# Optimization experiments

Hardware: AMD Instinct MI355X
Metric: run time of the kernel (lower is better)

The kernel has to match this reference:

```python
import jax, jax.numpy as jnp
import numpy as np

B, T, U = 64, 800, 96
VOCAB, CDIM, H, K, M = 80, 64, 400, 10, 20


def _lstm_cell(x, h, c, W_ih, W_hh, b_ih, b_hh):
    gates = x @ W_ih.T + h @ W_hh.T + b_ih + b_hh  # [B,4H]
    i, f, g, o = jnp.split(gates, 4, axis=-1)
    i, f, o = jax.nn.sigmoid(i), jax.nn.sigmoid(f), jax.nn.sigmoid(o)
    g = jnp.tanh(g)
    c = f * c + i * g
    h = o * jnp.tanh(c)
    return h, c


def setup_inputs() -> dict:
    key = jax.random.key(0)
    ks = jax.random.split(key, 16)
    s = 0.08
    emb = jax.random.normal(ks[0], (VOCAB, CDIM), jnp.float32) * s
    emb = emb.at[0].set(0.0)  # padding_idx=0
    d = {
        'x': jax.random.normal(ks[1], (B, T, 3), jnp.float32),
        'text_tokens': jax.random.randint(ks[2], (B, U), 0, VOCAB, jnp.int32),
        'emb': emb,
        'W_ih1': jax.random.normal(ks[3], (4 * H, 3 + CDIM), jnp.float32) * s,
        'W_hh1': jax.random.normal(ks[4], (4 * H, H), jnp.float32) * s,
        'b_ih1': jnp.zeros((4 * H,), jnp.float32),
        'b_hh1': jnp.zeros((4 * H,), jnp.float32),
        'W_ih2': jax.random.normal(ks[5], (4 * H, 3 + H + CDIM), jnp.float32) * s,
        'W_hh2': jax.random.normal(ks[6], (4 * H, H), jnp.float32) * s,
        'b_ih2': jnp.zeros((4 * H,), jnp.float32),
        'b_hh2': jnp.zeros((4 * H,), jnp.float32),
        'W_ih3': jax.random.normal(ks[7], (4 * H, 3 + H + CDIM), jnp.float32) * s,
        'W_hh3': jax.random.normal(ks[8], (4 * H, H), jnp.float32) * s,
        'b_ih3': jnp.zeros((4 * H,), jnp.float32),
        'b_hh3': jnp.zeros((4 * H,), jnp.float32),
        'W_w': jax.random.normal(ks[9], (3 * K, H), jnp.float32) * s,
        'b_w': jnp.concatenate([jnp.zeros((2 * K,), jnp.float32),
                                jnp.full((K,), -5.0, jnp.float32)]),
        'W_m': jax.random.normal(ks[10], (1 + 6 * M, 3 * H), jnp.float32) * s,
        'b_m': jnp.zeros((1 + 6 * M,), jnp.float32),
    }
    return d


def reference(x, text_tokens, emb, W_ih1, W_hh1, b_ih1, b_hh1,
              W_ih2, W_hh2, b_ih2, b_hh2, W_ih3, W_hh3, b_ih3, b_hh3,
              W_w, b_w, W_m, b_m):
    text_encoded = emb[text_tokens]  # [B,U,CDIM]
    u = jnp.arange(1, U + 1, dtype=jnp.float32)  # [U]

    z = jnp.zeros((B, H), jnp.float32)
    carry0 = (z, z, z, z, z, z,
              jnp.zeros((B, CDIM), jnp.float32),
              jnp.zeros((B, K), jnp.float32))

    def step(carry, x_t):
        h1, c1, h2, c2, h3, c3, w, kappa = carry
        h1, c1 = _lstm_cell(jnp.concatenate([x_t, w], -1), h1, c1,
                            W_ih1, W_hh1, b_ih1, b_hh1)
        # Gaussian window attention
        p = h1 @ W_w.T + b_w  # [B,3K]
        alpha_hat, beta_hat, kappa_hat = jnp.split(p, 3, axis=-1)
        alpha = jnp.exp(alpha_hat)
        beta = jnp.exp(beta_hat)
        kappa = kappa + jnp.exp(jnp.clip(kappa_hat, -10.0, 5.0))
        # phi: [B,U] = sum_k alpha * exp(-beta * (kappa - u)^2)
        diff = kappa[:, :, None] - u[None, None, :]  # [B,K,U]
        phi = jnp.sum(alpha[:, :, None] * jnp.exp(-beta[:, :, None] * diff * diff), axis=1)
        w = jnp.einsum('bu,bud->bd', phi, text_encoded)
        h2, c2 = _lstm_cell(jnp.concatenate([x_t, h1, w], -1), h2, c2,
                            W_ih2, W_hh2, b_ih2, b_hh2)
        h3, c3 = _lstm_cell(jnp.concatenate([x_t, h2, w], -1), h3, c3,
                            W_ih3, W_hh3, b_ih3, b_hh3)
        res = jnp.concatenate([h1, h2, h3], -1) @ W_m.T + b_m  # [B,1+6M]
        return (h1, c1, h2, c2, h3, c3, w, kappa), res

    _, res = jax.lax.scan(step, carry0, jnp.swapaxes(x, 0, 1))  # [T,B,1+6M]
    res = jnp.swapaxes(res, 0, 1)  # [B,T,1+6M]

    eos_hat = res[..., 0:1]
    pi = jax.nn.softmax(res[..., 1:1 + M], axis=-1)
    mu_x = res[..., 1 + M:1 + 2 * M]
    mu_y = res[..., 1 + 2 * M:1 + 3 * M]
    sigma_x = jnp.exp(res[..., 1 + 3 * M:1 + 4 * M]) + 1e-6
    sigma_y = jnp.exp(res[..., 1 + 4 * M:1 + 5 * M]) + 1e-6
    rho = jnp.tanh(res[..., 1 + 5 * M:1 + 6 * M]) * 0.999
    return (eos_hat, pi, mu_x, mu_y, sigma_x, sigma_y, rho)
```

## Files before the change

### kernel.cpp

```cpp
#include <hip/hip_runtime.h>


#define DI __device__ __forceinline__

typedef _Float16 f16;
typedef _Float16 f16x8 __attribute__((ext_vector_type(8)));
typedef _Float16 f16x4 __attribute__((ext_vector_type(4)));
typedef float f32x4 __attribute__((ext_vector_type(4)));
typedef unsigned long long u64;
typedef unsigned u32;

constexpr int Tn = 800, Un = 96, Hn = 400;
constexpr int P1 = 520, P2 = 904, P3 = 904, PM = 1288;
constexpr int NWG = 99;
constexpr int SP = 272;

constexpr size_t OFF_W1 = 0;
constexpr size_t SZ_W1 = (size_t)1600 * P1 * 2;
constexpr size_t OFF_W2 = OFF_W1 + SZ_W1;
constexpr size_t SZ_W2 = (size_t)1600 * P2 * 2;
constexpr size_t OFF_W3 = OFF_W2 + SZ_W2;
constexpr size_t OFF_WM = OFF_W3 + SZ_W2;
constexpr size_t SZ_WM = (size_t)128 * PM * 2;
constexpr size_t OFF_A1 = OFF_WM + SZ_WM;
constexpr size_t SZ_A1 = (size_t)2 * 64 * P1 * 2;
constexpr size_t OFF_A2 = OFF_A1 + SZ_A1;
constexpr size_t SZ_A2 = (size_t)2 * 64 * P2 * 2;
constexpr size_t OFF_A3 = OFF_A2 + SZ_A2;
constexpr size_t OFF_AM = OFF_A3 + SZ_A2;
constexpr size_t SZ_AM = (size_t)4 * 64 * PM * 2;
constexpr size_t OFF_TEB = OFF_AM + SZ_AM;
constexpr size_t SZ_TEB = (size_t)64 * 96 * 64 * 2;
constexpr size_t OFF_BS1 = OFF_TEB + SZ_TEB;
constexpr size_t OFF_BS2 = OFF_BS1 + 6400;
constexpr size_t OFF_BS3 = OFF_BS2 + 6400;
constexpr size_t OFF_BW = OFF_BS3 + 6400;
constexpr size_t OFF_BM = OFF_BW + 128;
constexpr size_t OFF_FLG = OFF_BM + 512;
constexpr size_t SZ_FLG = (size_t)808 * 5 * 16 * 4;
constexpr size_t OFF_PB = OFF_FLG + 24576;
constexpr size_t OFF_RES = OFF_FLG + SZ_FLG;

constexpr size_t O_EOS = 0, O_PI = 51200, O_MUX = 1075200, O_MUY = 2099200;
constexpr size_t O_SX = 3123200, O_SY = 4147200, O_RHO = 5171200;

constexpr int SB_L1 = 0;
constexpr int SB_ATT = 32;
constexpr int SB_L2 = 64;
constexpr int SB_L3 = 96;
constexpr int SB_OUT = 128;
constexpr int NSLOT = 160;

constexpr int GUARD_FLAG = 1200000;

DI u64 ldU8(const f16* p) {
  return __hip_atomic_load((const u64*)p, __ATOMIC_RELAXED, __HIP_MEMORY_SCOPE_AGENT);
}
DI void stU8(f16* p, u64 u) {
  __hip_atomic_store((u64*)p, u, __ATOMIC_RELAXED, __HIP_MEMORY_SCOPE_AGENT);
}
DI void stU8u(void* p, u64 u) {
  __hip_atomic_store((u64*)p, u, __ATOMIC_RELAXED, __HIP_MEMORY_SCOPE_AGENT);
}
DI u32 ldU4(const u32* p) {
  return __hip_atomic_load(p, __ATOMIC_RELAXED, __HIP_MEMORY_SCOPE_AGENT);
}
DI void stA4(f16* p, f16x4 v) {
  union { f16x4 v; u64 u; } c; c.v = v;
  stU8(p, c.u);
}
DI u64 pkf(float a, float b) {
  return (u64)__builtin_bit_cast(u32, a) | ((u64)__builtin_bit_cast(u32, b) << 32);
}

DI float sigm(float v) {
  return __builtin_amdgcn_rcpf(1.f + __expf(-v));
}
DI float ftanh(float v) {
  const float a = fabsf(v);
  const float e = __expf(-2.f * a);
  const float m = (1.f - e) * __builtin_amdgcn_rcpf(1.f + e);
  return v < 0.f ? -m : m;
}

DI void waitR(int* sl, int* doom,
              int b0, int n0, int q0, int b1, int n1, int q1,
              int b2, int n2, int q2, int b3, int n3, int q3) {
  if (!*doom) {
    if (threadIdx.x < 64) {
      const int l = (int)threadIdx.x;
      int sA = -1, qA = 0, sB = -1, qB = 0;
      {
        int idx = l;
        if (idx < n0) { sA = b0 + idx; qA = q0; }
        else { idx -= n0;
          if (idx < n1) { sA = b1 + idx; qA = q1; }
          else { idx -= n1;
            if (idx < n2) { sA = b2 + idx; qA = q2; }
            else { idx -= n2;
              if (idx < n3) { sA = b3 + idx; qA = q3; } } } }
      }
      {
        int idx = l + 64;
        if (idx < n0) { sB = b0 + idx; qB = q0; }
        else { idx -= n0;
          if (idx < n1) { sB = b1 + idx; qB = q1; }
          else { idx -= n1;
            if (idx < n2) { sB = b2 + idx; qB = q2; }
            else { idx -= n2;
              if (idx < n3) { sB = b3 + idx; qB = q3; } } } }
      }
      int okA = (sA < 0) ? 1 : 0, okB = (sB < 0) ? 1 : 0;
      int guard = 0;
      for (;;) {
        if (!okA)
          okA = (__hip_atomic_load(sl + sA * 32, __ATOMIC_RELAXED, __HIP_MEMORY_SCOPE_AGENT) >= qA) ? 1 : 0;
        if (!okB)
          okB = (__hip_atomic_load(sl + sB * 32, __ATOMIC_RELAXED, __HIP_MEMORY_SCOPE_AGENT) >= qB) ? 1 : 0;
        if (__all(okA & okB)) break;
        __builtin_amdgcn_s_sleep(1);
        if (++guard > GUARD_FLAG) { if (l == 0) *doom = 1; break; }
      }
    }
  }
  __syncthreads();
}
DI void arriveS(int* sl, int slot, int t) {
  __syncthreads();
  if (threadIdx.x == 0)
    __hip_atomic_store(sl + slot * 32, t, __ATOMIC_RELAXED, __HIP_MEMORY_SCOPE_AGENT);
}

template <int KN, int PITCH_>
DI void stage_ld(const f16* Ain, int tid, u64* lo, u64* hi) {
#pragma unroll
  for (int j = 0; j < KN; ++j) {
    const int i = tid + j * 256;
    const int r = i / (KN * 4), c16 = i % (KN * 4);
    const f16* p = Ain + (size_t)r * PITCH_ + c16 * 8;
    lo[j] = ldU8(p);
    hi[j] = ldU8(p + 4);
  }
}
template <int KN>
DI void stage_wr(f16* stg, int tid, const u64* lo, const u64* hi) {
#pragma unroll
  for (int j = 0; j < KN; ++j) {
    const int i = tid + j * 256;
    const int r = i / (KN * 4), c16 = i % (KN * 4);
    u64* q = (u64*)(stg + r * SP + c16 * 8);
    q[0] = lo[j];
    q[1] = hi[j];
  }
}
template <int KN>
DI void mfma_blk(const f16x8* wr, const f16* stg, int quad, int ln16, f32x4 acc[4]) {
#pragma unroll
  for (int ksl = 0; ksl < KN; ++ksl) {
    const int kc = ksl * 32 + quad * 8;
#pragma unroll
    for (int mt = 0; mt < 4; ++mt) {
      const f16x8 a = *(const f16x8*)(stg + (mt * 16 + ln16) * SP + kc);
      acc[mt] = __builtin_amdgcn_mfma_f32_16x16x32_f16(a, wr[ksl], acc[mt], 0, 0, 0);
    }
  }
}

DI void stage_ks14_ld(const f16* Ap, int pitch, const float* x, int t, int tid,
                      u64& sp, float& x0, float& x1, float& x2) {
  const int r = tid >> 2, cc = (tid & 3) * 4;
  sp = ldU8(Ap + (size_t)r * pitch + 448 + cc);
  if (tid < 64) {
    const float* xp = x + ((size_t)tid * Tn + t) * 3;
    x0 = xp[0]; x1 = xp[1]; x2 = xp[2];
  } else { x0 = x1 = x2 = 0.f; }
}
DI void stage_ks14_wr(f16* stg, int tid, u64 sp, float x0, float x1, float x2) {
  const int r = tid >> 2, cc = (tid & 3) * 4;
  *(u64*)(stg + r * SP + 128 + cc) = sp;
  if (tid < 64) {
    union { f16 h[4]; u64 u; } cx;
    cx.h[0] = (f16)x0; cx.h[1] = (f16)x1; cx.h[2] = (f16)x2; cx.h[3] = (f16)0.f;
    *(u64*)(stg + tid * SP + 144) = cx.u;
    *(u64*)(stg + tid * SP + 148) = 0ull;
    *(u64*)(stg + tid * SP + 152) = 0ull;
    *(u64*)(stg + tid * SP + 156) = 0ull;
  }
}

DI void gate_finish(f32x4 acc[4], float* red, float* cst, const float* bL, int tid,
                    int quad, int ln16, int wave,
                    f16* dA, int pA, f16* dB, int pB, f16* dC, int pC) {
#pragma unroll
  for (int mt = 0; mt < 4; ++mt)
#pragma unroll
    for (int r = 0; r < 4; ++r)
      red[wave * 1024 + (mt * 16 + quad * 4 + r) * 16 + ln16] = acc[mt][r];
  __syncthreads();
  {
    const int oi = tid * 4, b = oi >> 4, j0 = oi & 15;
    f32x4 gi = *(f32x4*)&red[oi];
    f32x4 gf = *(f32x4*)&red[1024 + oi];
    f32x4 gg = *(f32x4*)&red[2048 + oi];
    f32x4 go = *(f32x4*)&red[3072 + oi];
    f32x4 c = *(f32x4*)&cst[oi];
    f16x4 hv;
#pragma unroll
    for (int e = 0; e < 4; ++e) {
      const float iv = sigm(gi[e] + bL[j0 + e]);
      const float fv = sigm(gf[e] + bL[16 + j0 + e]);
      const float gv = ftanh(gg[e] + bL[32 + j0 + e]);
      const float ov = sigm(go[e] + bL[48 + j0 + e]);
      const float cn = fv * c[e] + iv * gv;
      c[e] = cn;
      hv[e] = (f16)(ov * ftanh(cn));
    }
    *(f32x4*)&cst[oi] = c;
    stA4(dA + b * pA + j0, hv);
    stA4(dB + b * pB + j0, hv);
    if (dC != nullptr) stA4(dC + b * pC + j0, hv);
  }
}

DI void gate_finish_l1(f32x4 acc[4], float* red, float* cst, const float* bL,
                       const float* wwL, int tid, int quad, int ln16, int wave,
                       u32* PBu, int jb,
                       f16* dA, int pA, f16* dB, int pB, f16* dC, int pC) {
#pragma unroll
  for (int mt = 0; mt < 4; ++mt)
#pragma unroll
    for (int r = 0; r < 4; ++r)
      red[wave * 1024 + (mt * 16 + quad * 4 + r) * 16 + ln16] = acc[mt][r];
  __syncthreads();
  const int oi = tid * 4, b = oi >> 4, j0 = oi & 15;
  f32x4 gi = *(f32x4*)&red[oi];
  f32x4 gf = *(f32x4*)&red[1024 + oi];
  f32x4 gg = *(f32x4*)&red[2048 + oi];
  f32x4 go = *(f32x4*)&red[3072 + oi];
  f32x4 c = *(f32x4*)&cst[oi];
  float hq[4];
  f16x4 hv;
#pragma unroll
  for (int e = 0; e < 4; ++e) {
    const float iv = sigm(gi[e] + bL[j0 + e]);
    const float fv = sigm(gf[e] + bL[16 + j0 + e]);
    const float gv = ftanh(gg[e] + bL[32 + j0 + e]);
    const float ov = sigm(go[e] + bL[48 + j0 + e]);
    const float cn = fv * c[e] + iv * gv;
    c[e] = cn;
    hq[e] = ov * ftanh(cn);
    hv[e] = (f16)hq[e];
  }
  *(f32x4*)&cst[oi] = c;
  float p[30];
#pragma unroll
  for (int r = 0; r < 30; ++r) {
    const f32x4 wv = *(const f32x4*)&wwL[r * 16 + j0];
    p[r] = wv[0] * hq[0] + wv[1] * hq[1] + wv[2] * hq[2] + wv[3] * hq[3];
  }
#pragma unroll
  for (int r = 0; r < 30; ++r) {
    p[r] += __shfl_xor(p[r], 1);
    p[r] += __shfl_xor(p[r], 2);
  }
  {
    const int s4 = tid & 3;
    u64* drow = (u64*)(PBu + (size_t)(jb * 64 + b) * 32);
    if (s4 == 0) {
      stU8u(drow + 0, pkf(p[0], p[1]));   stU8u(drow + 1, pkf(p[2], p[3]));
      stU8u(drow + 2, pkf(p[4], p[5]));   stU8u(drow + 3, pkf(p[6], p[7]));
    } else if (s4 == 1) {
      stU8u(drow + 4, pkf(p[8], p[9]));   stU8u(drow + 5, pkf(p[10], p[11]));
      stU8u(drow + 6, pkf(p[12], p[13])); stU8u(drow + 7, pkf(p[14], p[15]));
    } else if (s4 == 2) {
      stU8u(drow + 8, pkf(p[16], p[17])); stU8u(drow + 9, pkf(p[18], p[19]));
      stU8u(drow + 10, pkf(p[20], p[21])); stU8u(drow + 11, pkf(p[22], p[23]));
    } else {
      stU8u(drow + 12, pkf(p[24], p[25])); stU8u(drow + 13, pkf(p[26], p[27]));
      stU8u(drow + 14, pkf(p[28], p[29]));
    }
  }
  stA4(dA + b * pA + j0, hv);
  stA4(dB + b * pB + j0, hv);
  if (dC != nullptr) stA4(dC + b * pC + j0, hv);
}

DI void l1_role(char* ws, char* smem, int jb, const float* x, const float* Ww) {
  const int tid = threadIdx.x;
  const int wave = tid >> 6, lane = tid & 63, ln16 = lane & 15, quad = lane >> 4;
  const f16* W1 = (const f16*)(ws + OFF_W1);
  f16* A1 = (f16*)(ws + OFF_A1);
  f16* A2 = (f16*)(ws + OFF_A2);
  f16* AM = (f16*)(ws + OFF_AM);
  int* sl = (int*)(ws + OFF_FLG);
  u32* PBu = (u32*)(ws + OFF_PB);
  f16* stg = (f16*)smem;
  float* red = (float*)(smem + 34816);
  float* cst = (float*)(smem + 51200);
  float* bL = (float*)(smem + 55296);
  float* wwL = (float*)(smem + 55552);
  int* doom = (int*)(smem + 59384);
  const int row = wave * Hn + jb * 16 + ln16;
  f16x8 wr[16];
#pragma unroll
  for (int i = 0; i < 16; ++i) wr[i] = *(const f16x8*)(W1 + (size_t)row * P1 + i * 32 + quad * 8);
  if (tid < 64) bL[tid] = ((const float*)(ws + OFF_BS1))[(tid >> 4) * Hn + jb * 16 + (tid & 15)];
  for (int i = tid; i < 480; i += 256) {
    const int rr = i >> 4, jj = i & 15;
    wwL[i] = Ww[rr * 400 + jb * 16 + jj];
  }
  for (int z = tid; z < 1024; z += 256) cst[z] = 0.f;
  if (tid == 0) *doom = 0;
  __syncthreads();
  for (int t = 0; t < Tn; ++t) {
    const f16* Ap = A1 + (size_t)(t & 1) * 64 * P1;
    f32x4 acc[4];
#pragma unroll
    for (int mt = 0; mt < 4; ++mt) acc[mt] = f32x4{0.f, 0.f, 0.f, 0.f};
    waitR(sl, doom, SB_L1, 25, t - 1, SB_L2, 25, t - 2, SB_OUT, 8, t - 4, 0, 0, 0);
    u64 lo2[2], hi2[2];
    {
      u64 lo8[8], hi8[8], lo4[4], hi4[4], sp;
      float x0, x1, x2;
      stage_ld<8, P1>(Ap + 2 * 32, tid, lo8, hi8);
      stage_ld<4, P1>(Ap + 10 * 32, tid, lo4, hi4);
      stage_ks14_ld(Ap, P1, x, t, tid, sp, x0, x1, x2);
      stage_wr<8>(stg, tid, lo8, hi8);
      __syncthreads();
      mfma_blk<8>(wr + 2, stg, quad, ln16, acc);
      __syncthreads();
      stage_wr<4>(stg, tid, lo4, hi4);
      stage_ks14_wr(stg, tid, sp, x0, x1, x2);
      waitR(sl, doom, SB_ATT, 16, t - 1, 0, 0, 0, 0, 0, 0, 0, 0, 0);
      stage_ld<2, P1>(Ap + 0, tid, lo2, hi2);
      mfma_blk<4>(wr + 10, stg, quad, ln16, acc);
      mfma_blk<1>(wr + 14, stg + 128, quad, ln16, acc);
    }
    __syncthreads();
    stage_wr<2>(stg, tid, lo2, hi2);
    __syncthreads();
    mfma_blk<2>(wr + 0, stg, quad, ln16, acc);
    gate_finish_l1(acc, red, cst, bL, wwL, tid, quad, ln16, wave,
                   PBu, jb,
                   A1 + (size_t)((t + 1) & 1) * 64 * P1 + 64 + jb * 16, P1,
                   A2 + (size_t)(t & 1) * 64 * P2 + 64 + jb * 16, P2,
                   AM + (size_t)(t & 3) * 64 * PM + jb * 16, PM);
    arriveS(sl, SB_L1 + jb, t);
  }
}

DI void l2_role(char* ws, char* smem, int jb, const float* x) {
  const int tid = threadIdx.x;
  const int wave = tid >> 6, lane = tid & 63, ln16 = lane & 15, quad = lane >> 4;
  const f16* W2 = (const f16*)(ws + OFF_W2);
  f16* A2 = (f16*)(ws + OFF_A2);
  f16* A3 = (f16*)(ws + OFF_A3);
  f16* AM = (f16*)(ws + OFF_AM);
  int* sl = (int*)(ws + OFF_FLG);
  f16* stg = (f16*)smem;
  float* red = (float*)(smem + 34816);
  float* cst = (float*)(smem + 51200);
  float* bL = (float*)(smem + 55296);
  int* doom = (int*)(smem + 59384);
  const int row = wave * Hn + jb * 16 + ln16;
  f16x8 wr[28];
#pragma unroll
  for (int i = 0; i < 28; ++i) wr[i] = *(const f16x8*)(W2 + (size_t)row * P2 + i * 32 + quad * 8);
  if (tid < 64) bL[tid] = ((const float*)(ws + OFF_BS2))[(tid >> 4) * Hn + jb * 16 + (tid & 15)];
  for (int z = tid; z < 1024; z += 256) cst[z] = 0.f;
  if (tid == 0) *doom = 0;
  __syncthreads();
  for (int t = 0; t < Tn; ++t) {
    const f16* Ap = A2 + (size_t)(t & 1) * 64 * P2;
    f32x4 acc[4];
#pragma unroll
    for (int mt = 0; mt < 4; ++mt) acc[mt] = f32x4{0.f, 0.f, 0.f, 0.f};
    waitR(sl, doom, SB_L2, 25, t - 1, SB_L3, 25, t - 2, SB_OUT, 8, t - 4, 0, 0, 0);
    {
      u64 lo8[8], hi8[8], lo5[5], hi5[5];
      stage_ld<8, P2>(Ap + 15 * 32, tid, lo8, hi8);
      stage_ld<5, P2>(Ap + 23 * 32, tid, lo5, hi5);
      stage_wr<8>(stg, tid, lo8, hi8);
      __syncthreads();
      mfma_blk<8>(wr + 15, stg, quad, ln16, acc);
      __syncthreads();
      stage_wr<5>(stg, tid, lo5, hi5);
      __syncthreads();
      mfma_blk<5>(wr + 23, stg, quad, ln16, acc);
    }
    waitR(sl, doom, SB_L1, 25, t, 0, 0, 0, 0, 0, 0, 0, 0, 0);
    u64 lo2[2], hi2[2];
    {
      u64 lo8[8], hi8[8], lo4[4], hi4[4], sp;
      float x0, x1, x2;
      stage_ld<8, P2>(Ap + 2 * 32, tid, lo8, hi8);
      stage_ld<4, P2>(Ap + 10 * 32, tid, lo4, hi4);
      stage_ks14_ld(Ap, P2, x, t, tid, sp, x0, x1, x2);
      stage_wr<8>(stg, tid, lo8, hi8);
      __syncthreads();
      mfma_blk<8>(wr + 2, stg, quad, ln16, acc);
      __syncthreads();
      stage_wr<4>(stg, tid, lo4, hi4);
      stage_ks14_wr(stg, tid, sp, x0, x1, x2);
      waitR(sl, doom, SB_ATT, 16, t, 0, 0, 0, 0, 0, 0, 0, 0, 0);
      stage_ld<2, P2>(Ap + 0, tid, lo2, hi2);
      mfma_blk<4>(wr + 10, stg, quad, ln16, acc);
      mfma_blk<1>(wr + 14, stg + 128, quad, ln16, acc);
    }
    __syncthreads();
    stage_wr<2>(stg, tid, lo2, hi2);
    __syncthreads();
    mfma_blk<2>(wr + 0, stg, quad, ln16, acc);
    gate_finish(acc, red, cst, bL, tid, quad, ln16, wave,
                A2 + (size_t)((t + 1) & 1) * 64 * P2 + 480 + jb * 16, P2,
                A3 + (size_t)(t & 1) * 64 * P3 + 64 + jb * 16, P3,
                AM + (size_t)(t & 3) * 64 * PM + Hn + jb * 16, PM);
    arriveS(sl, SB_L2 + jb, t);
  }
}

DI void l3_role(char* ws, char* smem, int jb, const float* x) {
  const int tid = threadIdx.x;
  const int wave = tid >> 6, lane = tid & 63, ln16 = lane & 15, quad = lane >> 4;
  const f16* W3 = (const f16*)(ws + OFF_W3);
  f16* A3 = (f16*)(ws + OFF_A3);
  f16* AM = (f16*)(ws + OFF_AM);
  int* sl = (int*)(ws + OFF_FLG);
  f16* stg = (f16*)smem;
  float* red = (float*)(smem + 34816);
  float* cst = (float*)(smem + 51200);
  float* bL = (float*)(smem + 55296);
  int* doom = (int*)(smem + 59384);
  const int row = wave * Hn + jb * 16 + ln16;
  f16x8 wr[28];
#pragma unroll
  for (int i = 0; i < 28; ++i) wr[i] = *(const f16x8*)(W3 + (size_t)row * P2 + i * 32 + quad * 8);
  if (tid < 64) bL[tid] = ((const float*)(ws + OFF_BS3))[(tid >> 4) * Hn + jb * 16 + (tid & 15)];
  for (int z = tid; z < 1024; z += 256) cst[z] = 0.f;
  if (tid == 0) *doom = 0;
  __syncthreads();
  for (int t = 0; t < Tn; ++t) {
    const f16* Ap = A3 + (size_t)(t & 1) * 64 * P3;
    f32x4 acc[4];
#pragma unroll
    for (int mt = 0; mt < 4; ++mt) acc[mt] = f32x4{0.f, 0.f, 0.f, 0.f};
    waitR(sl, doom, SB_L3, 25, t - 1, SB_OUT, 8, t - 4, 0, 0, 0, 0, 0, 0);
    {
      u64 lo8[8], hi8[8], lo5[5], hi5[5];
      stage_ld<8, P3>(Ap + 15 * 32, tid, lo8, hi8);
      stage_ld<5, P3>(Ap + 23 * 32, tid, lo5, hi5);
      stage_wr<8>(stg, tid, lo8, hi8);
      __syncthreads();
      mfma_blk<8>(wr + 15, stg, quad, ln16, acc);
      __syncthreads();
      stage_wr<5>(stg, tid, lo5, hi5);
      __syncthreads();
      mfma_blk<5>(wr + 23, stg, quad, ln16, acc);
    }
    waitR(sl, doom, SB_L2, 25, t, 0, 0, 0, 0, 0, 0, 0, 0, 0);
    u64 lo2[2], hi2[2];
    {
      u64 lo8[8], hi8[8], lo4[4], hi4[4], sp;
      float x0, x1, x2;
      stage_ld<8, P3>(Ap + 2 * 32, tid, lo8, hi8);
      stage_ld<4, P3>(Ap + 10 * 32, tid, lo4, hi4);
      stage_ks14_ld(Ap, P3, x, t, tid, sp, x0, x1, x2);
      stage_wr<8>(stg, tid, lo8, hi8);
      __syncthreads();
      mfma_blk<8>(wr + 2, stg, quad, ln16, acc);
      __syncthreads();
      stage_wr<4>(stg, tid, lo4, hi4);
      stage_ks14_wr(stg, tid, sp, x0, x1, x2);
      waitR(sl, doom, SB_ATT, 16, t, 0, 0, 0, 0, 0, 0, 0, 0, 0);
      stage_ld<2, P3>(Ap + 0, tid, lo2, hi2);
      mfma_blk<4>(wr + 10, stg, quad, ln16, acc);
      mfma_blk<1>(wr + 14, stg + 128, quad, ln16, acc);
    }
    __syncthreads();
    stage_wr<2>(stg, tid, lo2, hi2);
    __syncthreads();
    mfma_blk<2>(wr + 0, stg, quad, ln16, acc);
    gate_finish(acc, red, cst, bL, tid, quad, ln16, wave,
                A3 + (size_t)((t + 1) & 1) * 64 * P3 + 480 + jb * 16, P3,
                AM + (size_t)(t & 3) * 64 * PM + 2 * Hn + jb * 16, PM,
                nullptr, 0);
    arriveS(sl, SB_L3 + jb, t);
  }
}

DI void att_role(char* ws, char* smem, int ab) {
  const int tid = threadIdx.x;
  const int b0 = ab * 4;
  f16* A1 = (f16*)(ws + OFF_A1);
  f16* A2 = (f16*)(ws + OFF_A2);
  f16* A3 = (f16*)(ws + OFF_A3);
  int* sl = (int*)(ws + OFF_FLG);
  const u32* PBu = (const u32*)(ws + OFF_PB);
  f16* tebL = (f16*)smem;
  float* aL = (float*)(smem + 49152);
  float* beL = (float*)(smem + 49312);
  float* kaL = (float*)(smem + 49472);
  float* phiL = (float*)(smem + 49632);
  float* bwL = (float*)(smem + 51168);
  f16* wL = (f16*)(smem + 51296);
  int* doom = (int*)(smem + 59384);
  for (int i = tid; i < 24576; i += 256)
    tebL[i] = ((const f16*)(ws + OFF_TEB))[(size_t)b0 * 6144 + i];
  if (tid < 40) kaL[tid] = 0.f;
  if (tid < 30) bwL[tid] = ((const float*)(ws + OFF_BW))[tid];
  if (tid == 0) *doom = 0;
  __syncthreads();
  const int bl = tid / 30, r = tid % 30;
  const bool act = tid < 120;
  const u32* pbase = PBu + (size_t)(b0 + (act ? bl : 0)) * 32 + (act ? r : 0);
  for (int t = 0; t < Tn; ++t) {
    waitR(sl, doom, SB_L1, 25, t, SB_L2, 25, t - 2, SB_L3, 25, t - 2, 0, 0, 0);
    if (act) {
      float s = bwL[r];
#pragma unroll
      for (int jb = 0; jb < 25; ++jb)
        s += __builtin_bit_cast(float, ldU4(pbase + jb * 2048));
      if (r < 10) aL[bl * 10 + r] = __expf(s);
      else if (r < 20) beL[bl * 10 + r - 10] = __expf(s);
      else kaL[bl * 10 + r - 20] += __expf(fminf(5.f, fmaxf(-10.f, s)));
    }
    __syncthreads();
    for (int idx = tid; idx < 384; idx += 256) {
      const int b = idx / 96;
      const float u1 = (float)(idx % 96 + 1);
      float s2 = 0.f;
#pragma unroll
      for (int k = 0; k < 10; ++k) {
        const float d = kaL[b * 10 + k] - u1;
        s2 += aL[b * 10 + k] * __expf(-beL[b * 10 + k] * d * d);
      }
      phiL[idx] = s2;
    }
    __syncthreads();
    {
      const int b = tid >> 6, d = tid & 63;
      float wv0 = 0.f, wv1 = 0.f;
      for (int u = 0; u < 48; ++u) {
        wv0 += phiL[b * 96 + u] * (float)tebL[(b * 96 + u) * 64 + d];
        wv1 += phiL[b * 96 + 48 + u] * (float)tebL[(b * 96 + 48 + u) * 64 + d];
      }
      wL[tid] = (f16)(wv0 + wv1);
    }
    __syncthreads();
    if (tid < 64) {
      const u64 wq = ((u64*)wL)[tid];
      const int bg = b0 + (tid >> 4), d0 = (tid & 15) * 4;
      stU8(A1 + (size_t)((t + 1) & 1) * 64 * P1 + bg * P1 + d0, wq);
      stU8(A2 + (size_t)(t & 1) * 64 * P2 + bg * P2 + d0, wq);
      stU8(A3 + (size_t)(t & 1) * 64 * P3 + bg * P3 + d0, wq);
    }
    arriveS(sl, SB_ATT + ab, t);
  }
}

template <int KN>
DI void out_chunk(const f16* Ap, const f16x8* wm, f16* stg, int tid, int wave,
                  int quad, int ln16, f32x4& acc) {
  u64 lo[KN], hi[KN];
#pragma unroll
  for (int j = 0; j < KN; ++j) {
    const int i = tid + j * 256;
    const int r = i / (KN * 4), c16 = i % (KN * 4);
    const f16* p = Ap + (size_t)r * PM + c16 * 8;
    lo[j] = ldU8(p);
    hi[j] = ldU8(p + 4);
  }
  __syncthreads();
#pragma unroll
  for (int j = 0; j < KN; ++j) {
    const int i = tid + j * 256;
    const int r = i / (KN * 4), c16 = i % (KN * 4);
    u64* q = (u64*)(stg + r * SP + c16 * 8);
    q[0] = lo[j];
    q[1] = hi[j];
  }
  __syncthreads();
#pragma unroll
  for (int ksl = 0; ksl < KN; ++ksl) {
    const f16x8 a = *(const f16x8*)(stg + (wave * 16 + ln16) * SP + ksl * 32 + quad * 8);
    acc = __builtin_amdgcn_mfma_f32_16x16x32_f16(a, wm[ksl], acc, 0, 0, 0);
  }
}

DI void out_role(char* ws, char* smem, int nt) {
  const int tid = threadIdx.x;
  const int wave = tid >> 6, lane = tid & 63, ln16 = lane & 15, quad = lane >> 4;
  const f16* WM = (const f16*)(ws + OFF_WM);
  const f16* AM = (const f16*)(ws + OFF_AM);
  float* resb = (float*)(ws + OFF_RES);
  int* sl = (int*)(ws + OFF_FLG);
  f16* stg = (f16*)smem;
  float* bmL = (float*)(smem + 34816);
  int* doom = (int*)(smem + 59384);
  f16x8 wm[38];
#pragma unroll
  for (int i = 0; i < 38; ++i)
    wm[i] = *(const f16x8*)(WM + (size_t)(nt * 16 + ln16) * PM + i * 32 + quad * 8);
  if (tid < 16) bmL[tid] = ((const float*)(ws + OFF_BM))[nt * 16 + tid];
  if (tid == 0) *doom = 0;
  __syncthreads();

  for (int t = 0; t < Tn; ++t) {
    waitR(sl, doom, SB_L1, 25, t, SB_L2, 25, t, SB_L3, 25, t, 0, 0, 0);
    const f16* Ap = AM + (size_t)(t & 3) * 64 * PM;
    f32x4 acc = f32x4{0.f, 0.f, 0.f, 0.f};
    out_chunk<8>(Ap + 0 * 32, wm + 0, stg, tid, wave, quad, ln16, acc);
    out_chunk<8>(Ap + 8 * 32, wm + 8, stg, tid, wave, quad, ln16, acc);
    out_chunk<8>(Ap + 16 * 32, wm + 16, stg, tid, wave, quad, ln16, acc);
    out_chunk<8>(Ap + 24 * 32, wm + 24, stg, tid, wave, quad, ln16, acc);
    out_chunk<6>(Ap + 32 * 32, wm + 32, stg, tid, wave, quad, ln16, acc);
#pragma unroll
    for (int e = 0; e < 4; ++e) {
      const int m = wave * 16 + quad * 4 + e;
      resb[((size_t)t * 64 + m) * 128 + nt * 16 + ln16] = acc[e] + bmL[ln16];
    }
    arriveS(sl, SB_OUT + nt, t);
  }
}

__global__ void __launch_bounds__(256, 1) coop_kernel(char* ws, const float* x, const float* Ww) {
  __shared__ char smem[59392];
  const int id = (int)blockIdx.x;
  if (id < 25) l1_role(ws, smem, id, x, Ww);
  else if (id < 50) l2_role(ws, smem, id - 25, x);
  else if (id < 75) l3_role(ws, smem, id - 50, x);
  else if (id < 91) att_role(ws, smem, id - 75);
  else out_role(ws, smem, id - 91);
}

__global__ void init_build(char* ws, const int* tok, const float* emb,
                           const float* Wih1, const float* Whh1, const float* bih1, const float* bhh1,
                           const float* Wih2, const float* Whh2, const float* bih2, const float* bhh2,
                           const float* Wih3, const float* Whh3, const float* bih3, const float* bhh3,
                           const float* bw, const float* Wm, const float* bm) {
  const int blk = (int)blockIdx.x, tid = (int)threadIdx.x;
  if (blk < 1600) {
    const int j = blk;
    f16* W1 = (f16*)(ws + OFF_W1) + (size_t)j * P1;
    f16* W2 = (f16*)(ws + OFF_W2) + (size_t)j * P2;
    f16* W3 = (f16*)(ws + OFF_W3) + (size_t)j * P2;
    for (int c = tid; c < P1; c += 256) {
      float v = 0.f;
      if (c < 64) v = Wih1[(size_t)j * 67 + 3 + c];
      else if (c < 464) v = Whh1[(size_t)j * 400 + c - 64];
      else if (c < 467) v = Wih1[(size_t)j * 67 + c - 464];
      W1[c] = (f16)v;
    }
    for (int c = tid; c < P2; c += 256) {
      float v2 = 0.f, v3 = 0.f;
      if (c < 64) { v2 = Wih2[(size_t)j * 467 + 403 + c]; v3 = Wih3[(size_t)j * 467 + 403 + c]; }
      else if (c < 464) { v2 = Wih2[(size_t)j * 467 + 3 + c - 64]; v3 = Wih3[(size_t)j * 467 + 3 + c - 64]; }
      else if (c < 467) { v2 = Wih2[(size_t)j * 467 + c - 464]; v3 = Wih3[(size_t)j * 467 + c - 464]; }
      else if (c >= 480 && c < 880) { v2 = Whh2[(size_t)j * 400 + c - 480]; v3 = Whh3[(size_t)j * 400 + c - 480]; }
      W2[c] = (f16)v2;
      W3[c] = (f16)v3;
    }
  } else if (blk < 1728) {
    const int r = blk - 1600;
    f16* WMp = (f16*)(ws + OFF_WM) + (size_t)r * PM;
    for (int c = tid; c < PM; c += 256) {
      const float v = (r < 121 && c < 1200) ? Wm[(size_t)r * 1200 + c] : 0.f;
      WMp[c] = (f16)v;
    }
  } else if (blk == 1728) {
    float* bs1 = (float*)(ws + OFF_BS1);
    float* bs2 = (float*)(ws + OFF_BS2);
    float* bs3 = (float*)(ws + OFF_BS3);
    for (int i = tid; i < 1600; i += 256) {
      bs1[i] = bih1[i] + bhh1[i];
      bs2[i] = bih2[i] + bhh2[i];
      bs3[i] = bih3[i] + bhh3[i];
    }
    float* bwp = (float*)(ws + OFF_BW);
    if (tid < 32) bwp[tid] = (tid < 30) ? bw[tid] : 0.f;
    float* bmp = (float*)(ws + OFF_BM);
    if (tid < 128) bmp[tid] = (tid < 121) ? bm[tid] : 0.f;
  } else if (blk == 1729) {
    int* fl = (int*)(ws + OFF_FLG);
    for (int i = tid; i < NSLOT; i += 256) fl[i * 32] = -1;
  } else if (blk < 1762) {
    unsigned* az = (unsigned*)(ws + OFF_A1);
    const int n = (int)((SZ_A1 + 2 * SZ_A2 + SZ_AM) / 4);
    for (int i = (blk - 1730) * 256 + tid; i < n; i += 32 * 256) az[i] = 0u;
  } else {
    f16* tebp = (f16*)(ws + OFF_TEB);
    const int n = 64 * 96 * 64;
    for (int i = (blk - 1762) * 256 + tid; i < n; i += 128 * 256) {
      const int b = i / (96 * 64);
      const int rem = i % (96 * 64);
      const int u = rem >> 6, d = rem & 63;
      const int tk = tok[b * 96 + u];
      tebp[i] = (f16)emb[(size_t)tk * 64 + d];
    }
  }
}

__global__ void postproc(const char* ws, float* out) {
  __shared__ float r[50 * 128];
  __shared__ float mx[50], dn[50];
  const float* resb = (const float*)(ws + OFF_RES);
  const int tid = (int)threadIdx.x;
  const int b = (int)blockIdx.x >> 4;
  const int t0 = ((int)blockIdx.x & 15) * 50;
  for (int idx = tid; idx < 50 * 128; idx += 256) {
    const int tt = idx >> 7, c = idx & 127;
    r[idx] = resb[((size_t)(t0 + tt) * 64 + b) * 128 + c];
  }
  __syncthreads();
  if (tid < 50) {
    float m = -1e30f;
    for (int k = 0; k < 20; ++k) m = fmaxf(m, r[tid * 128 + 1 + k]);
    float s = 0.f;
    for (int k = 0; k < 20; ++k) s += expf(r[tid * 128 + 1 + k] - m);
    mx[tid] = m;
    dn[tid] = 1.f / s;
  }
  __syncthreads();
  for (int idx = tid; idx < 50; idx += 256)
    out[O_EOS + (size_t)b * Tn + t0 + idx] = r[idx * 128];
  for (int idx = tid; idx < 50 * 20; idx += 256) {
    const int tt = idx / 20, k = idx % 20;
    const size_t o = ((size_t)b * Tn + t0 + tt) * 20 + k;
    const float* rr = &r[tt * 128];
    out[O_PI + o] = expf(rr[1 + k] - mx[tt]) * dn[tt];
    out[O_MUX + o] = rr[21 + k];
    out[O_MUY + o] = rr[41 + k];
    out[O_SX + o] = expf(rr[61 + k]) + 1e-6f;
    out[O_SY + o] = expf(rr[81 + k]) + 1e-6f;
    out[O_RHO + o] = tanhf(rr[101 + k]) * 0.999f;
  }
}

extern "C" void kernel_launch(void* const* d_in, const int* in_sizes, int n_in,
                              void* d_out, int out_size, void* d_ws, size_t ws_size,
                              hipStream_t stream) {
  const float* x = (const float*)d_in[0];
  const int* tok = (const int*)d_in[1];
  const float* emb = (const float*)d_in[2];
  const float* Wih1 = (const float*)d_in[3];
  const float* Whh1 = (const float*)d_in[4];
  const float* bih1 = (const float*)d_in[5];
  const float* bhh1 = (const float*)d_in[6];
  const float* Wih2 = (const float*)d_in[7];
  const float* Whh2 = (const float*)d_in[8];
  const float* bih2 = (const float*)d_in[9];
  const float* bhh2 = (const float*)d_in[10];
  const float* Wih3 = (const float*)d_in[11];
  const float* Whh3 = (const float*)d_in[12];
  const float* bih3 = (const float*)d_in[13];
  const float* bhh3 = (const float*)d_in[14];
  const float* Ww = (const float*)d_in[15];
  const float* bw = (const float*)d_in[16];
  const float* Wm = (const float*)d_in[17];
  const float* bm = (const float*)d_in[18];
  char* ws = (char*)d_ws;
  float* out = (float*)d_out;

  hipLaunchKernelGGL(init_build, dim3(1890), dim3(256), 0, stream,
                     ws, tok, emb, Wih1, Whh1, bih1, bhh1, Wih2, Whh2, bih2, bhh2,
                     Wih3, Whh3, bih3, bhh3, bw, Wm, bm);

  hipLaunchKernelGGL(coop_kernel, dim3(NWG), dim3(256), 0, stream, ws, x, Ww);

  hipLaunchKernelGGL(postproc, dim3(1024), dim3(256), 0, stream, ws, out);
}
```

Before: 6.672 ms.

## Make attention role per-wave with per-batch flags, removing block barriers

The attention role now runs each wave independently on one batch row. Each wave reduces the partial window parameters, computes phi and the attention vector using wave shuffles instead of shared memory and __syncthreads, then publishes its own per-batch flag. The flag layout is widened from 16 attention slots to 64, so consumer layers now wait on 64 flags instead of 16. This removes block-wide barriers from the attention step on the critical recurrent path, at the cost of more flag polling for consumers. A pitch typo in the W3 load is also corrected (P2 and P3 are equal, so it has no effect).

Result: slower. 9.015 ms (+35.1%).

```diff
diff --git a/kernel.cpp b/kernel.cpp
--- a/kernel.cpp
+++ b/kernel.cpp
@@ -46,10 +46,10 @@
 
 constexpr int SB_L1 = 0;
 constexpr int SB_ATT = 32;
-constexpr int SB_L2 = 64;
-constexpr int SB_L3 = 96;
-constexpr int SB_OUT = 128;
-constexpr int NSLOT = 160;
+constexpr int SB_L2 = 96;
+constexpr int SB_L3 = 128;
+constexpr int SB_OUT = 160;
+constexpr int NSLOT = 168;
 
 constexpr int GUARD_FLAG = 1200000;
 
@@ -131,6 +131,40 @@
     __hip_atomic_store(sl + slot * 32, t, __ATOMIC_RELAXED, __HIP_MEMORY_SCOPE_AGENT);
 }
 
+DI void waitW(int* sl, int* doom, int lane,
+              int b0, int n0, int q0, int b1, int n1, int q1,
+              int b2, int n2, int q2) {
+  if (*doom) return;
+  int sA = -1, qA = 0, sB = -1, qB = 0;
+  {
+    int idx = lane;
+    if (idx < n0) { sA = b0 + idx; qA = q0; }
+    else { idx -= n0;
+      if (idx < n1) { sA = b1 + idx; qA = q1; }
+      else { idx -= n1;
+        if (idx < n2) { sA = b2 + idx; qA = q2; } } }
+  }
+  {
+    int idx = lane + 64;
+    if (idx < n0) { sB = b0 + idx; qB = q0; }
+    else { idx -= n0;
+      if (idx < n1) { sB = b1 + idx; qB = q1; }
+      else { idx -= n1;
+        if (idx < n2) { sB = b2 + idx; qB = q2; } } }
+  }
+  int okA = (sA < 0) ? 1 : 0, okB = (sB < 0) ? 1 : 0;
+  int guard = 0;
+  for (;;) {
+    if (!okA)
+      okA = (__hip_atomic_load(sl + sA * 32, __ATOMIC_RELAXED, __HIP_MEMORY_SCOPE_AGENT) >= qA) ? 1 : 0;
+    if (!okB)
+      okB = (__hip_atomic_load(sl + sB * 32, __ATOMIC_RELAXED, __HIP_MEMORY_SCOPE_AGENT) >= qB) ? 1 : 0;
+    if (__all(okA & okB)) break;
+    __builtin_amdgcn_s_sleep(1);
+    if (++guard > GUARD_FLAG) { if (lane == 0) *doom = 1; break; }
+  }
+}
+
 template <int KN, int PITCH_>
 DI void stage_ld(const f16* Ain, int tid, u64* lo, u64* hi) {
 #pragma unroll
@@ -331,7 +365,7 @@
       __syncthreads();
       stage_wr<4>(stg, tid, lo4, hi4);
       stage_ks14_wr(stg, tid, sp, x0, x1, x2);
-      waitR(sl, doom, SB_ATT, 16, t - 1, 0, 0, 0, 0, 0, 0, 0, 0, 0);
+      waitR(sl, doom, SB_ATT, 64, t - 1, 0, 0, 0, 0, 0, 0, 0, 0, 0);
       stage_ld<2, P1>(Ap + 0, tid, lo2, hi2);
       mfma_blk<4>(wr + 10, stg, quad, ln16, acc);
       mfma_blk<1>(wr + 14, stg + 128, quad, ln16, acc);
@@ -402,7 +436,7 @@
       __syncthreads();
       stage_wr<4>(stg, tid, lo4, hi4);
       stage_ks14_wr(stg, tid, sp, x0, x1, x2);
-      waitR(sl, doom, SB_ATT, 16, t, 0, 0, 0, 0, 0, 0, 0, 0, 0);
+      waitR(sl, doom, SB_ATT, 64, t, 0, 0, 0, 0, 0, 0, 0, 0, 0);
       stage_ld<2, P2>(Ap + 0, tid, lo2, hi2);
       mfma_blk<4>(wr + 10, stg, quad, ln16, acc);
       mfma_blk<1>(wr + 14, stg + 128, quad, ln16, acc);
@@ -434,7 +468,7 @@
   const int row = wave * Hn + jb * 16 + ln16;
   f16x8 wr[28];
 #pragma unroll
-  for (int i = 0; i < 28; ++i) wr[i] = *(const f16x8*)(W3 + (size_t)row * P2 + i * 32 + quad * 8);
+  for (int i = 0; i < 28; ++i) wr[i] = *(const f16x8*)(W3 + (size_t)row * P3 + i * 32 + quad * 8);
   if (tid < 64) bL[tid] = ((const float*)(ws + OFF_BS3))[(tid >> 4) * Hn + jb * 16 + (tid & 15)];
   for (int z = tid; z < 1024; z += 256) cst[z] = 0.f;
   if (tid == 0) *doom = 0;
@@ -471,7 +505,7 @@
       __syncthreads();
       stage_wr<4>(stg, tid, lo4, hi4);
       stage_ks14_wr(stg, tid, sp, x0, x1, x2);
-      waitR(sl, doom, SB_ATT, 16, t, 0, 0, 0, 0, 0, 0, 0, 0, 0);
+      waitR(sl, doom, SB_ATT, 64, t, 0, 0, 0, 0, 0, 0, 0, 0, 0);
       stage_ld<2, P3>(Ap + 0, tid, lo2, hi2);
       mfma_blk<4>(wr + 10, stg, quad, ln16, acc);
       mfma_blk<1>(wr + 14, stg + 128, quad, ln16, acc);
@@ -490,71 +524,76 @@
 
 DI void att_role(char* ws, char* smem, int ab) {
   const int tid = threadIdx.x;
-  const int b0 = ab * 4;
+  const int wave = tid >> 6, lane = tid & 63;
+  const int bb = ab * 4 + wave;
   f16* A1 = (f16*)(ws + OFF_A1);
   f16* A2 = (f16*)(ws + OFF_A2);
   f16* A3 = (f16*)(ws + OFF_A3);
   int* sl = (int*)(ws + OFF_FLG);
   const u32* PBu = (const u32*)(ws + OFF_PB);
   f16* tebL = (f16*)smem;
-  float* aL = (float*)(smem + 49152);
-  float* beL = (float*)(smem + 49312);
-  float* kaL = (float*)(smem + 49472);
-  float* phiL = (float*)(smem + 49632);
-  float* bwL = (float*)(smem + 51168);
-  f16* wL = (f16*)(smem + 51296);
+  float* phiL = (float*)(smem + 49152);
+  float* bwL = (float*)(smem + 50688);
   int* doom = (int*)(smem + 59384);
   for (int i = tid; i < 24576; i += 256)
-    tebL[i] = ((const f16*)(ws + OFF_TEB))[(size_t)b0 * 6144 + i];
-  if (tid < 40) kaL[tid] = 0.f;
+    tebL[i] = ((const f16*)(ws + OFF_TEB))[(size_t)(ab * 4) * 6144 + i];
   if (tid < 30) bwL[tid] = ((const float*)(ws + OFF_BW))[tid];
   if (tid == 0) *doom = 0;
   __syncthreads();
-  const int bl = tid / 30, r = tid % 30;
-  const bool act = tid < 120;
-  const u32* pbase = PBu + (size_t)(b0 + (act ? bl : 0)) * 32 + (act ? r : 0);
+  const f16* tebW = tebL + wave * 6144;
+  float* phiW = phiL + wave * 96;
+  float kareg = 0.f;
+  const u32* prow = PBu + (size_t)bb * 32 + (lane >> 1);
+  const int jh = lane & 1;
+  const float u0f = (float)(lane + 1), u1f = (float)(lane + 65);
   for (int t = 0; t < Tn; ++t) {
-    waitR(sl, doom, SB_L1, 25, t, SB_L2, 25, t - 2, SB_L3, 25, t - 2, 0, 0, 0);
-    if (act) {
-      float s = bwL[r];
-#pragma unroll
-      for (int jb = 0; jb < 25; ++jb)
-        s += __builtin_bit_cast(float, ldU4(pbase + jb * 2048));
-      if (r < 10) aL[bl * 10 + r] = __expf(s);
-      else if (r < 20) beL[bl * 10 + r - 10] = __expf(s);
-      else kaL[bl * 10 + r - 20] += __expf(fminf(5.f, fmaxf(-10.f, s)));
-    }
-    __syncthreads();
-    for (int idx = tid; idx < 384; idx += 256) {
-      const int b = idx / 96;
-      const float u1 = (float)(idx % 96 + 1);
-      float s2 = 0.f;
-#pragma unroll
-      for (int k = 0; k < 10; ++k) {
-        const float d = kaL[b * 10 + k] - u1;
-        s2 += aL[b * 10 + k] * __expf(-beL[b * 10 + k] * d * d);
-      }
-      phiL[idx] = s2;
-    }
-    __syncthreads();
-    {
-      const int b = tid >> 6, d = tid & 63;
-      float wv0 = 0.f, wv1 = 0.f;
-      for (int u = 0; u < 48; ++u) {
-        wv0 += phiL[b * 96 + u] * (float)tebL[(b * 96 + u) * 64 + d];
-        wv1 += phiL[b * 96 + 48 + u] * (float)tebL[(b * 96 + 48 + u) * 64 + d];
-      }
-      wL[tid] = (f16)(wv0 + wv1);
-    }
-    __syncthreads();
-    if (tid < 64) {
-      const u64 wq = ((u64*)wL)[tid];
-      const int bg = b0 + (tid >> 4), d0 = (tid & 15) * 4;
-      stU8(A1 + (size_t)((t + 1) & 1) * 64 * P1 + bg * P1 + d0, wq);
-      stU8(A2 + (size_t)(t & 1) * 64 * P2 + bg * P2 + d0, wq);
-      stU8(A3 + (size_t)(t & 1) * 64 * P3 + bg * P3 + d0, wq);
-    }
-    arriveS(sl, SB_ATT + ab, t);
+    waitW(sl, doom, lane, SB_L1, 25, t, SB_L2, 25, t - 2, SB_L3, 25, t - 2);
+    float s = 0.f;
+    if (lane < 60) {
+      const int j0 = jh * 13, jn = jh ? 12 : 13;
+      for (int j = 0; j < jn; ++j)
+        s += __builtin_bit_cast(float, ldU4(prow + (size_t)(j0 + j) * 2048));
+    }
+    s += __shfl_xor(s, 1);
+    float rowv = __shfl(s, lane * 2);
+    float ex = 0.f;
+    if (lane < 30) {
+      rowv += bwL[lane];
+      if (lane < 20) ex = __expf(rowv);
+      else { kareg += __expf(fminf(5.f, fmaxf(-10.f, rowv))); ex = kareg; }
+    }
+    float phi0 = 0.f, phi1 = 0.f;
+#pragma unroll
+    for (int k = 0; k < 10; ++k) {
+      const float a = __shfl(ex, k);
+      const float be = __shfl(ex, 10 + k);
+      const float ka = __shfl(ex, 20 + k);
+      const float d0 = ka - u0f;
+      phi0 += a * __expf(-be * d0 * d0);
+      const float d1 = ka - u1f;
+      phi1 += a * __expf(-be * d1 * d1);
+    }
+    phiW[lane] = phi0;
+    if (lane < 32) phiW[64 + lane] = phi1;
+    asm volatile("s_waitcnt lgkmcnt(0)" ::: "memory");
+    float wv = 0.f;
+    for (int u = 0; u < 96; ++u)
+      wv += phiW[u] * (float)tebW[u * 64 + lane];
+    const u32 m = (u32)__builtin_bit_cast(unsigned short, (f16)wv);
+    const u32 m0 = __shfl(m, lane * 4);
+    const u32 m1 = __shfl(m, lane * 4 + 1);
+    const u32 m2 = __shfl(m, lane * 4 + 2);
+    const u32 m3 = __shfl(m, lane * 4 + 3);
+    if (lane < 16) {
+      const u64 wq = (u64)m0 | ((u64)m1 << 16) | ((u64)m2 << 32) | ((u64)m3 << 48);
+      const int d0 = lane * 4;
+      stU8(A1 + (size_t)((t + 1) & 1) * 64 * P1 + (size_t)bb * P1 + d0, wq);
+      stU8(A2 + (size_t)(t & 1) * 64 * P2 + (size_t)bb * P2 + d0, wq);
+      stU8(A3 + (size_t)(t & 1) * 64 * P3 + (size_t)bb * P3 + d0, wq);
+    }
+    asm volatile("s_waitcnt vmcnt(0)" ::: "memory");
+    if (lane == 0)
+      __hip_atomic_store(sl + (SB_ATT + bb) * 32, t, __ATOMIC_RELAXED, __HIP_MEMORY_SCOPE_AGENT);
   }
 }
 
```
